# Kernel optimization log

Measured on AMD Instinct MI355X. Metric: run time of the kernel, lower is better.

## Reference

```python
import jax, jax.numpy as jnp
import numpy as np

FRAME, PROJ, MID, HID, T, B = 2048, 512, 128, 1024, 48, 512


def _uniform(key, shape, stdv):
    return jax.random.uniform(key, shape, jnp.float32, -stdv, stdv)


def setup_inputs() -> dict:
    key = jax.random.key(0)
    ks = jax.random.split(key, 16)
    sp = 1.0 / np.sqrt(FRAME)   # frame_embed init
    s1 = 1.0 / np.sqrt(HID)     # LSTMCell init (1/sqrt(hidden))
    sbd = 1.0 / np.sqrt(PROJ)   # BoundaryDetector init (1/sqrt(i_features))
    return {
        "video_feats": jax.random.normal(ks[0], (B, T, FRAME), jnp.float32),
        # frame_embed: Linear(frame_size, projected_size)
        "We": _uniform(ks[1], (PROJ, FRAME), sp),
        "be": _uniform(ks[2], (PROJ,), sp),
        # lstm1: LSTMCell(projected, hidden) with bias
        "W1_ih": _uniform(ks[3], (4 * HID, PROJ), s1),
        "W1_hh": _uniform(ks[4], (4 * HID, HID), s1),
        "b1_ih": _uniform(ks[5], (4 * HID,), s1),
        "b1_hh": _uniform(ks[6], (4 * HID,), s1),
        # lstm2: LSTMCell(hidden, hidden), bias=False
        "W2_ih": _uniform(ks[7], (4 * HID, HID), s1),
        "W2_hh": _uniform(ks[8], (4 * HID, HID), s1),
        # BoundaryDetector params
        "Wsi": _uniform(ks[9], (MID, PROJ), sbd),
        "Wsh": _uniform(ks[10], (MID, HID), sbd),
        "bbd": _uniform(ks[11], (MID,), sbd),
        "vs": _uniform(ks[12], (1, MID), sbd),
    }


def _lstm_cell(x, h, c, W_ih, W_hh, b):
    gates = x @ W_ih.T + h @ W_hh.T + b  # [B, 4H]
    i, f, g, o = jnp.split(gates, 4, axis=-1)  # PyTorch gate order i,f,g,o
    i, f, o = jax.nn.sigmoid(i), jax.nn.sigmoid(f), jax.nn.sigmoid(o)
    g = jnp.tanh(g)
    c_new = f * c + i * g
    h_new = o * jnp.tanh(c_new)
    return h_new, c_new


def _binary_gate(z):
    # eval mode: threshold 0.5; straight-through identity backward
    hard = (z > 0.5).astype(z.dtype)
    return z + jax.lax.stop_gradient(hard - z)


def reference(video_feats, We, be, W1_ih, W1_hh, b1_ih, b1_hh, W2_ih, W2_hh, Wsi, Wsh, bbd, vs):
    bsz = video_feats.shape[0]
    # frame embedding (dropout is identity in eval mode)
    v = video_feats @ We.T + be  # [B, T, PROJ]
    v_t = jnp.swapaxes(v, 0, 1)  # [T, B, PROJ]
    b1 = b1_ih + b1_hh
    zeros = jnp.zeros((bsz, HID), video_feats.dtype)

    def step(carry, vt):
        h1, c1, h2, c2 = carry
        z = jax.nn.sigmoid((vt @ Wsi.T + h1 @ Wsh.T + bbd) @ vs.T)  # [B, 1]
        s = _binary_gate(z)
        h1n, c1n = _lstm_cell(vt, h1, c1, W1_ih, W1_hh, b1)
        h2n, c2n = _lstm_cell(h1n * s, h2, c2, W2_ih, W2_hh, 0.0)
        h1n = h1n * (1.0 - s)
        c1n = c1n * (1.0 - s)
        return (h1n, c1n, h2n, c2n), None

    (h1, _, _, _), _ = jax.lax.scan(step, (zeros, zeros, zeros, zeros), v_t)
    return h1
```

## Files before the change

kernel.cpp:

```cpp
#include <hip/hip_runtime.h>

#define B_     512
#define T_     48
#define FRAME_ 2048
#define PROJ_  512
#define MID_   128
#define HID_   1024
#define G4_    4096

typedef unsigned short u16;
typedef __bf16 bf16x8 __attribute__((ext_vector_type(8)));
typedef float  f32x4  __attribute__((ext_vector_type(4)));

__device__ __forceinline__ float sigmoidf_(float x) {
    return 1.0f / (1.0f + expf(-x));
}
__device__ __forceinline__ u16 f2bf_rn(float f) {
    unsigned int u = __float_as_uint(f);
    u += 0x7fffu + ((u >> 16) & 1u);
    return (u16)(u >> 16);
}
__device__ __forceinline__ float bf2f(u16 s) {
    return __uint_as_float(((unsigned int)s) << 16);
}
__device__ __forceinline__ void gld16(const void* g, void* l) {
    __builtin_amdgcn_global_load_lds((const __attribute__((address_space(1))) void*)g,
                                     (__attribute__((address_space(3))) void*)l, 16, 0, 0);
}
__device__ __forceinline__ uint4 pack8(const u16* h) {
    return make_uint4((unsigned)h[0] | ((unsigned)h[1] << 16),
                      (unsigned)h[2] | ((unsigned)h[3] << 16),
                      (unsigned)h[4] | ((unsigned)h[5] << 16),
                      (unsigned)h[6] | ((unsigned)h[7] << 16));
}

__global__ void wvec_kernel(const float* __restrict__ Wsi, const float* __restrict__ Wsh,
                            const float* __restrict__ vs,
                            double* __restrict__ wsi_vd, float* __restrict__ wsh_v)
{
    const int gid = blockIdx.x * 256 + threadIdx.x;
    if (gid < 512) {
        double s = 0.0;
        for (int mi = 0; mi < MID_; ++mi)
            s += (double)vs[mi] * (double)Wsi[(size_t)mi * PROJ_ + gid];
        wsi_vd[gid] = s;
    } else if (gid < 1536) {
        const int k = gid - 512;
        double s = 0.0;
        for (int mi = 0; mi < MID_; ++mi)
            s += (double)vs[mi] * (double)Wsh[(size_t)mi * HID_ + k];
        wsh_v[k] = (float)s;
    }
}

__global__ void cc_kernel(const float* __restrict__ be, const double* __restrict__ wsi_vd,
                          const float* __restrict__ vs, const float* __restrict__ bbd,
                          double* __restrict__ cc)
{
    __shared__ double red[256];
    const int tid = threadIdx.x;
    double s = 0.0;
    for (int p = tid; p < PROJ_; p += 256) s += (double)be[p] * wsi_vd[p];
    red[tid] = s;
    __syncthreads();
    for (int st = 128; st > 0; st >>= 1) {
        if (tid < st) red[tid] += red[tid + st];
        __syncthreads();
    }
    if (tid == 0) {
        double b = 0.0;
        for (int mi = 0; mi < MID_; ++mi) b += (double)vs[mi] * (double)bbd[mi];
        cc[0] = red[0] + b;
    }
}

__global__ void u_kernel(const float* __restrict__ We, const double* __restrict__ wsi_vd,
                         double* __restrict__ u)
{
    const int f = blockIdx.x * 256 + threadIdx.x;
    double s = 0.0;
    for (int p = 0; p < PROJ_; ++p)
        s += wsi_vd[p] * (double)We[(size_t)p * FRAME_ + f];
    u[f] = s;
}

__global__ __launch_bounds__(256)
void vidpack_kernel(const float* __restrict__ video, const double* __restrict__ u,
                    const double* __restrict__ cc,
                    u16* __restrict__ phi, u16* __restrict__ plo,
                    float* __restrict__ Lv)
{
    __shared__ double red[16][17];
    const int tid = threadIdx.x;
    const int r   = tid & 15, kq = tid >> 4;
    const int row = blockIdx.x * 16 + r;
    const float* vr = video + (size_t)row * FRAME_;
    double s = 0.0;
#pragma unroll
    for (int j = 0; j < 16; ++j) {
        const int k0 = kq * 128 + j * 8;
        const float4 a = *(const float4*)&vr[k0];
        const float4 b = *(const float4*)&vr[k0 + 4];
        const float f[8] = {a.x, a.y, a.z, a.w, b.x, b.y, b.z, b.w};
        s += (double)f[0]*u[k0+0] + (double)f[1]*u[k0+1] + (double)f[2]*u[k0+2]
           + (double)f[3]*u[k0+3] + (double)f[4]*u[k0+4] + (double)f[5]*u[k0+5]
           + (double)f[6]*u[k0+6] + (double)f[7]*u[k0+7];
        u16 h[8], l[8];
#pragma unroll
        for (int e = 0; e < 8; ++e) {
            h[e] = f2bf_rn(f[e]);
            l[e] = f2bf_rn(f[e] - bf2f(h[e]));
        }
        const int g = kq * 16 + j;
        const size_t off = ((size_t)g * 24576 + row) * 16;
        *(uint4*)((char*)phi + off) = pack8(h);
        *(uint4*)((char*)plo + off) = pack8(l);
    }
    red[r][kq] = s;
    __syncthreads();
    if (tid < 16) {
        double t = 0.0;
#pragma unroll
        for (int q = 0; q < 16; ++q) t += red[tid][q];
        const int rw = blockIdx.x * 16 + tid;
        Lv[(rw % T_) * B_ + rw / T_] = (float)(t + cc[0]);
    }
}

__global__ void wepack_kernel(const float* __restrict__ We,
                              u16* __restrict__ phi, u16* __restrict__ plo)
{
    const int kk = blockIdx.x, by = blockIdx.y, tid = threadIdx.x;
#pragma unroll
    for (int pass = 0; pass < 2; ++pass) {
        const int g = tid + pass * 256;
        const int ko = g >> 7, n = g & 127;
        const int p = by * 128 + n;
        const int k = kk * 32 + ko * 8;
        const float4 a = *(const float4*)&We[(size_t)p * FRAME_ + k];
        const float4 b = *(const float4*)&We[(size_t)p * FRAME_ + k + 4];
        const float f[8] = {a.x, a.y, a.z, a.w, b.x, b.y, b.z, b.w};
        u16 h[8], l[8];
#pragma unroll
        for (int e = 0; e < 8; ++e) {
            h[e] = f2bf_rn(f[e]);
            l[e] = f2bf_rn(f[e] - bf2f(h[e]));
        }
        const size_t off = (((size_t)by * 64 + kk) * 512 + g) * 16;
        *(uint4*)((char*)phi + off) = pack8(h);
        *(uint4*)((char*)plo + off) = pack8(l);
    }
}

__global__ void wpack_kernel(const float* __restrict__ Wih, const float* __restrict__ Whh,
                             u16* __restrict__ phi, u16* __restrict__ plo)
{
    const int kk = blockIdx.x, by = blockIdx.y, tid = threadIdx.x;
#pragma unroll
    for (int pass = 0; pass < 2; ++pass) {
        const int g = tid + pass * 256;
        const int ko = g >> 7, n = g & 127;
        const int gate = n & 3, hl = n >> 2;
        const int srow = gate * HID_ + by * 32 + hl;
        const int k = kk * 32 + ko * 8;
        float4 a, b;
        if (k < 512) {
            a = *(const float4*)&Wih[(size_t)srow * PROJ_ + k];
            b = *(const float4*)&Wih[(size_t)srow * PROJ_ + k + 4];
        } else {
            a = *(const float4*)&Whh[(size_t)srow * HID_ + (k - 512)];
            b = *(const float4*)&Whh[(size_t)srow * HID_ + (k - 508)];
        }
        const float f[8] = {a.x, a.y, a.z, a.w, b.x, b.y, b.z, b.w};
        u16 h[8], l[8];
#pragma unroll
        for (int e = 0; e < 8; ++e) {
            h[e] = f2bf_rn(f[e]);
            l[e] = f2bf_rn(f[e] - bf2f(h[e]));
        }
        const size_t off = (((size_t)by * 48 + kk) * 512 + g) * 16;
        *(uint4*)((char*)phi + off) = pack8(h);
        *(uint4*)((char*)plo + off) = pack8(l);
    }
}

__global__ __launch_bounds__(512, 1)
void embed_mfma_kernel(const u16* __restrict__ Ahi_g, const u16* __restrict__ Alo_g,
                       const u16* __restrict__ Bhi_g, const u16* __restrict__ Blo_g,
                       const float* __restrict__ be,
                       u16* __restrict__ vphi, u16* __restrict__ vplo)
{
    __shared__ char smem[73728];
    const int tid = threadIdx.x;
    const int u_ = (blockIdx.x & 7) * 192 + (blockIdx.x >> 3);
    const int by = u_ / 384, bx = u_ % 384;
    const int n0 = by * 128;
    const int w = tid >> 6, l = tid & 63, lm = l & 15, ko4 = l >> 4;
    const int wr = (w >> 2) * 32, wc = (w & 3) * 32;
    const int t8 = tid & 255;
    const int koA = t8 >> 6, am = t8 & 63;

    const char* aV = (const char*)(tid < 256 ? Ahi_g : Alo_g)
                     + (size_t)koA * 393216 + ((size_t)bx * 64 + am) * 16;
    const char* bh = (const char*)Bhi_g + (size_t)by * 524288 + tid * 16;
    const char* bl = (const char*)Blo_g + (size_t)by * 524288 + tid * 16;

    auto stage = [&](int s, int buf) {
        char* base = smem + buf * 24576;
        gld16(aV + (size_t)s * 1572864, base + (tid >> 8) * 4096 + t8 * 16);
        gld16(bh + (size_t)s * 8192, base + 8192 + tid * 16);
        gld16(bl + (size_t)s * 8192, base + 16384 + tid * 16);
    };

    f32x4 acc[2][2] = {};
    stage(0, 0);
    stage(1, 1);
    for (int kk = 0; kk < 64; ++kk) {
        const int cb = kk % 3;
        if (kk + 2 < 64) {
            stage(kk + 2, (kk + 2) % 3);
            asm volatile("s_waitcnt vmcnt(6)" ::: "memory");
        } else if (kk + 1 < 64) {
            asm volatile("s_waitcnt vmcnt(3)" ::: "memory");
        } else {
            asm volatile("s_waitcnt vmcnt(0)" ::: "memory");
        }
        __builtin_amdgcn_sched_barrier(0);
        __builtin_amdgcn_s_barrier();

        const char* rb = smem + cb * 24576;
        bf16x8 fAh[2], fAl[2], fBh[2], fBl[2];
#pragma unroll
        for (int mt = 0; mt < 2; ++mt) {
            const int idx = ko4 * 64 + wr + mt * 16 + lm;
            fAh[mt] = *(const bf16x8*)(rb + idx * 16);
            fAl[mt] = *(const bf16x8*)(rb + 4096 + idx * 16);
        }
#pragma unroll
        for (int nt = 0; nt < 2; ++nt) {
            const int idx = ko4 * 128 + wc + nt * 16 + lm;
            fBh[nt] = *(const bf16x8*)(rb + 8192 + idx * 16);
            fBl[nt] = *(const bf16x8*)(rb + 16384 + idx * 16);
        }
        asm volatile("s_waitcnt lgkmcnt(0)" ::: "memory");
        __builtin_amdgcn_sched_barrier(0);
        __builtin_amdgcn_s_barrier();
        __builtin_amdgcn_s_setprio(1);
#pragma unroll
        for (int mt = 0; mt < 2; ++mt)
#pragma unroll
            for (int nt = 0; nt < 2; ++nt) {
                acc[mt][nt] = __builtin_amdgcn_mfma_f32_16x16x32_bf16(fAh[mt], fBh[nt], acc[mt][nt], 0, 0, 0);
                acc[mt][nt] = __builtin_amdgcn_mfma_f32_16x16x32_bf16(fAh[mt], fBl[nt], acc[mt][nt], 0, 0, 0);
                acc[mt][nt] = __builtin_amdgcn_mfma_f32_16x16x32_bf16(fAl[mt], fBh[nt], acc[mt][nt], 0, 0, 0);
            }
        __builtin_amdgcn_s_setprio(0);
    }

    __syncthreads();
    float* S = (float*)smem;
#pragma unroll
    for (int mt = 0; mt < 2; ++mt)
#pragma unroll
        for (int nt = 0; nt < 2; ++nt) {
            const int col = wc + nt * 16 + lm;
#pragma unroll
            for (int r = 0; r < 4; ++r) {
                const int row = wr + mt * 16 + ko4 * 4 + r;
                S[row * 132 + col] = acc[mt][nt][r];
            }
        }
    __syncthreads();

#pragma unroll
    for (int pass = 0; pass < 2; ++pass) {
        const int pidx = tid + pass * 512;
        const int m = pidx >> 4, gr = pidx & 15;
        const int p0 = n0 + gr * 8;
        const float4 s0 = *(const float4*)&S[m * 132 + gr * 8];
        const float4 s1 = *(const float4*)&S[m * 132 + gr * 8 + 4];
        const float4 e0 = *(const float4*)&be[p0];
        const float4 e1 = *(const float4*)&be[p0 + 4];
        const float o[8] = {s0.x + e0.x, s0.y + e0.y, s0.z + e0.z, s0.w + e0.w,
                            s1.x + e1.x, s1.y + e1.y, s1.z + e1.z, s1.w + e1.w};
        u16 h[8], lo[8];
#pragma unroll
        for (int e = 0; e < 8; ++e) {
            h[e] = f2bf_rn(o[e]);
            lo[e] = f2bf_rn(o[e] - bf2f(h[e]));
        }
        const int R = bx * 64 + m;
        const int t = R % T_, b = R / T_;
        const size_t off = (size_t)t * 524288 + (((size_t)(p0 >> 3)) * 512 + b) * 16;
        *(uint4*)((char*)vphi + off) = pack8(h);
        *(uint4*)((char*)vplo + off) = pack8(lo);
    }
}

__global__ __launch_bounds__(512, 1)
void lstm_mfma_kernel(const u16* __restrict__ vthi, const u16* __restrict__ vtlo,
                      const u16* __restrict__ hhi,  const u16* __restrict__ hlo,
                      const u16* __restrict__ Whi,  const u16* __restrict__ Wlo,
                      const float* __restrict__ b1,
                      const float* __restrict__ Lv_t,
                      const float* __restrict__ Pin,
                      float* __restrict__ Pout,
                      const float* __restrict__ wsh_v,
                      float* __restrict__ c1, float* __restrict__ h1o,
                      u16* __restrict__ hhio, u16* __restrict__ hloo)
{
    __shared__ char smem[73984];
    float* keepsm = (float*)(smem + 73728);
    const int tid = threadIdx.x;
    const int bid = blockIdx.x;
    const int xcd = bid & 7, slot = bid >> 3;
    const int by  = xcd * 4 + (slot & 3);
    const int bx  = slot >> 2;
    const int b0  = bx * 64;
    const int w = tid >> 6, l = tid & 63, lm = l & 15, ko4 = l >> 4;
    const int wr = (w >> 2) * 32, wc = (w & 3) * 32;
    const int t8 = tid & 255;
    const int koA = t8 >> 6, am = t8 & 63;

    const char* aV = (const char*)(tid < 256 ? vthi : vtlo)
                     + koA * 8192 + (b0 + am) * 16;
    const char* aH = (const char*)(tid < 256 ? hhi : hlo)
                     + koA * 8192 + (b0 + am) * 16;
    const char* bh = (const char*)Whi + (size_t)by * 393216 + tid * 16;
    const char* bl = (const char*)Wlo + (size_t)by * 393216 + tid * 16;

    auto stage = [&](int s, int buf) {
        char* base = smem + buf * 24576;
        const char* asrc = (s < 16) ? aV + s * 32768 : aH + (s - 16) * 32768;
        gld16(asrc, base + (tid >> 8) * 4096 + t8 * 16);
        gld16(bh + s * 8192, base + 8192 + tid * 16);
        gld16(bl + s * 8192, base + 16384 + tid * 16);
    };

    f32x4 acc[2][2] = {};
    stage(0, 0);
    stage(1, 1);

    if (tid < 64) {
        double s = (double)Lv_t[b0 + tid];
#pragma unroll
        for (int j = 0; j < 32; ++j) s += (double)Pin[j * B_ + b0 + tid];
        keepsm[tid] = (s > 0.0) ? 0.0f : 1.0f;
    }

    for (int kk = 0; kk < 48; ++kk) {
        const int cb = kk % 3;
        if (kk + 2 < 48) {
            stage(kk + 2, (kk + 2) % 3);
            asm volatile("s_waitcnt vmcnt(6)" ::: "memory");
        } else if (kk + 1 < 48) {
            asm volatile("s_waitcnt vmcnt(3)" ::: "memory");
        } else {
            asm volatile("s_waitcnt vmcnt(0)" ::: "memory");
        }
        __builtin_amdgcn_sched_barrier(0);
        __builtin_amdgcn_s_barrier();

        const char* rb = smem + cb * 24576;
        bf16x8 fAh[2], fAl[2], fBh[2], fBl[2];
#pragma unroll
        for (int mt = 0; mt < 2; ++mt) {
            const int idx = ko4 * 64 + wr + mt * 16 + lm;
            fAh[mt] = *(const bf16x8*)(rb + idx * 16);
            fAl[mt] = *(const bf16x8*)(rb + 4096 + idx * 16);
        }
#pragma unroll
        for (int nt = 0; nt < 2; ++nt) {
            const int idx = ko4 * 128 + wc + nt * 16 + lm;
            fBh[nt] = *(const bf16x8*)(rb + 8192 + idx * 16);
            fBl[nt] = *(const bf16x8*)(rb + 16384 + idx * 16);
        }
        asm volatile("s_waitcnt lgkmcnt(0)" ::: "memory");
        __builtin_amdgcn_sched_barrier(0);
        __builtin_amdgcn_s_barrier();
        __builtin_amdgcn_s_setprio(1);
#pragma unroll
        for (int mt = 0; mt < 2; ++mt)
#pragma unroll
            for (int nt = 0; nt < 2; ++nt) {
                acc[mt][nt] = __builtin_amdgcn_mfma_f32_16x16x32_bf16(fAh[mt], fBh[nt], acc[mt][nt], 0, 0, 0);
                acc[mt][nt] = __builtin_amdgcn_mfma_f32_16x16x32_bf16(fAh[mt], fBl[nt], acc[mt][nt], 0, 0, 0);
                acc[mt][nt] = __builtin_amdgcn_mfma_f32_16x16x32_bf16(fAl[mt], fBh[nt], acc[mt][nt], 0, 0, 0);
            }
        __builtin_amdgcn_s_setprio(0);
    }

    __syncthreads();
    float* S = (float*)smem;
#pragma unroll
    for (int mt = 0; mt < 2; ++mt)
#pragma unroll
        for (int nt = 0; nt < 2; ++nt) {
            const int col = wc + nt * 16 + lm;
#pragma unroll
            for (int r = 0; r < 4; ++r) {
                const int row = wr + mt * 16 + ko4 * 4 + r;
                S[row * 132 + col] = acc[mt][nt][r];
            }
        }
    __syncthreads();

    const int h_l = tid & 31, rg = tid >> 5;
    const int hg  = by * 32 + h_l;
    const float bI = b1[hg], bF = b1[HID_ + hg], bG = b1[2 * HID_ + hg], bO = b1[3 * HID_ + hg];
    const float wv = wsh_v[hg];
    const size_t hgbase = (((size_t)by * 4 + (h_l >> 3)) * 512) * 16 + (h_l & 7) * 2;
#pragma unroll
    for (int i = 0; i < 4; ++i) {
        const int m = rg * 4 + i;
        const int b = b0 + m;
        const float4 g4 = *(const float4*)&S[m * 132 + h_l * 4];
        const float i_ = sigmoidf_(g4.x + bI);
        const float f_ = sigmoidf_(g4.y + bF);
        const float g_ = tanhf(g4.z + bG);
        const float o_ = sigmoidf_(g4.w + bO);
        const size_t off = (size_t)b * HID_ + hg;
        float cn = f_ * c1[off] + i_ * g_;
        float hn = o_ * tanhf(cn);
        const float kp = keepsm[m];
        cn *= kp; hn *= kp;
        c1[off] = cn;
        if (h1o) h1o[off] = hn;
        const u16 hb = f2bf_rn(hn);
        const size_t hoff = hgbase + (size_t)b * 16;
        *(u16*)((char*)hhio + hoff) = hb;
        *(u16*)((char*)hloo + hoff) = f2bf_rn(hn - bf2f(hb));
        float pr = hn * wv;
        pr += __shfl_xor(pr, 16);
        pr += __shfl_xor(pr, 8);
        pr += __shfl_xor(pr, 4);
        pr += __shfl_xor(pr, 2);
        pr += __shfl_xor(pr, 1);
        if (h_l == 0) Pout[by * B_ + b] = pr;
    }
}

__global__ void b1sum_kernel(const float* __restrict__ bih,
                             const float* __restrict__ bhh,
                             float* __restrict__ b1)
{
    const int i = blockIdx.x * 256 + threadIdx.x;
    if (i < G4_) b1[i] = bih[i] + bhh[i];
}

extern "C" void kernel_launch(void* const* d_in, const int* in_sizes, int n_in,
                              void* d_out, int out_size, void* d_ws, size_t ws_size,
                              hipStream_t stream)
{
    const float* video = (const float*)d_in[0];
    const float* We    = (const float*)d_in[1];
    const float* be    = (const float*)d_in[2];
    const float* W1_ih = (const float*)d_in[3];
    const float* W1_hh = (const float*)d_in[4];
    const float* b1_ih = (const float*)d_in[5];
    const float* b1_hh = (const float*)d_in[6];
    const float* Wsi   = (const float*)d_in[9];
    const float* Wsh   = (const float*)d_in[10];
    const float* bbd   = (const float*)d_in[11];
    const float* vs    = (const float*)d_in[12];
    float* out = (float*)d_out;

    char* p = (char*)d_ws;
    auto alloc = [&](size_t bytes) { char* r = p; p += (bytes + 255) & ~(size_t)255; return r; };
    u16* vidhi = (u16*)alloc((size_t)24576 * FRAME_ * 2);
    u16* vidlo = (u16*)alloc((size_t)24576 * FRAME_ * 2);
    u16* vphi  = (u16*)alloc((size_t)T_ * B_ * PROJ_ * 2);
    u16* vplo  = (u16*)alloc((size_t)T_ * B_ * PROJ_ * 2);
    u16* Wehi  = (u16*)alloc((size_t)PROJ_ * FRAME_ * 2);
    u16* Welo  = (u16*)alloc((size_t)PROJ_ * FRAME_ * 2);
    u16* Whi   = (u16*)alloc((size_t)G4_ * 1536 * 2);
    u16* Wlo   = (u16*)alloc((size_t)G4_ * 1536 * 2);
    float* c1  = (float*)alloc((size_t)B_ * HID_ * 4);
    u16* hhiA  = (u16*)alloc((size_t)B_ * HID_ * 2);
    u16* hhiB  = (u16*)alloc((size_t)B_ * HID_ * 2);
    u16* hloA  = (u16*)alloc((size_t)B_ * HID_ * 2);
    u16* hloB  = (u16*)alloc((size_t)B_ * HID_ * 2);
    double* wsi_vd = (double*)alloc(512 * 8);
    double* ud     = (double*)alloc(2048 * 8);
    double* ccd    = (double*)alloc(256);
    float* wsh_v = (float*)alloc(1024 * 4);
    float* Lv    = (float*)alloc((size_t)T_ * B_ * 4);
    float* PA    = (float*)alloc(32 * B_ * 4);
    float* PB    = (float*)alloc(32 * B_ * 4);
    float* b1    = (float*)alloc(G4_ * 4);

    hipMemsetAsync(c1,   0, (size_t)B_ * HID_ * 4, stream);
    hipMemsetAsync(hhiA, 0, (size_t)B_ * HID_ * 2, stream);
    hipMemsetAsync(hloA, 0, (size_t)B_ * HID_ * 2, stream);
    hipMemsetAsync(PA,   0, 32 * B_ * 4, stream);

    b1sum_kernel<<<16, 256, 0, stream>>>(b1_ih, b1_hh, b1);
    wvec_kernel<<<6, 256, 0, stream>>>(Wsi, Wsh, vs, wsi_vd, wsh_v);
    cc_kernel<<<1, 256, 0, stream>>>(be, wsi_vd, vs, bbd, ccd);
    u_kernel<<<8, 256, 0, stream>>>(We, wsi_vd, ud);
    wepack_kernel<<<dim3(64, 4), 256, 0, stream>>>(We, Wehi, Welo);
    wpack_kernel<<<dim3(48, 32), 256, 0, stream>>>(W1_ih, W1_hh, Whi, Wlo);
    vidpack_kernel<<<1536, 256, 0, stream>>>(video, ud, ccd, vidhi, vidlo, Lv);
    embed_mfma_kernel<<<1536, 512, 0, stream>>>(vidhi, vidlo, Wehi, Welo, be, vphi, vplo);

    u16* hhi_in = hhiA; u16* hhi_out = hhiB;
    u16* hlo_in = hloA; u16* hlo_out = hloB;
    float* Pin = PA; float* Pout = PB;

    for (int t = 0; t < T_; ++t) {
        const u16* vthi = vphi + (size_t)t * 262144;
        const u16* vtlo = vplo + (size_t)t * 262144;
        float* ho = (t == T_ - 1) ? out : nullptr;
        lstm_mfma_kernel<<<256, 512, 0, stream>>>(vthi, vtlo, hhi_in, hlo_in,
                                                  Whi, Wlo, b1,
                                                  Lv + t * B_, Pin, Pout, wsh_v,
                                                  c1, ho, hhi_out, hlo_out);
        { u16* tmp = hhi_in; hhi_in = hhi_out; hhi_out = tmp; }
        { u16* tmp = hlo_in; hlo_in = hlo_out; hlo_out = tmp; }
        { float* tmp = Pin; Pin = Pout; Pout = tmp; }
    }
}
```

Baseline: 1.699 ms.

## Hoist input-to-hidden LSTM projection out of recurrence into one batched GEMM

Splits the LSTM weight packing into separate W_ih and W_hh buffers and adds a gx_mfma kernel that computes x_t·W_ih^T plus bias for all 48 timesteps at once into a large fp32 Gx buffer. Each recurrent step then runs only the 1024-deep hidden GEMM and adds the precomputed Gx slice in the epilogue. The aim is to move a third of the serial per-step work into one highly parallel GEMM, at the cost of about 400 MB of extra Gx writes and reads. The embed and LSTM pipelines are also changed to issue the next stage load after the fragment reads and to drop one barrier per iteration, and the embed block-to-tile mapping is changed.

```diff
diff --git a/kernel.cpp b/kernel.cpp
--- a/kernel.cpp
+++ b/kernel.cpp
@@ -152,8 +152,8 @@
     }
 }
 
-__global__ void wpack_kernel(const float* __restrict__ Wih, const float* __restrict__ Whh,
-                             u16* __restrict__ phi, u16* __restrict__ plo)
+__global__ void wihpack_kernel(const float* __restrict__ Wih,
+                               u16* __restrict__ phi, u16* __restrict__ plo)
 {
     const int kk = blockIdx.x, by = blockIdx.y, tid = threadIdx.x;
 #pragma unroll
@@ -163,14 +163,8 @@
         const int gate = n & 3, hl = n >> 2;
         const int srow = gate * HID_ + by * 32 + hl;
         const int k = kk * 32 + ko * 8;
-        float4 a, b;
-        if (k < 512) {
-            a = *(const float4*)&Wih[(size_t)srow * PROJ_ + k];
-            b = *(const float4*)&Wih[(size_t)srow * PROJ_ + k + 4];
-        } else {
-            a = *(const float4*)&Whh[(size_t)srow * HID_ + (k - 512)];
-            b = *(const float4*)&Whh[(size_t)srow * HID_ + (k - 508)];
-        }
+        const float4 a = *(const float4*)&Wih[(size_t)srow * PROJ_ + k];
+        const float4 b = *(const float4*)&Wih[(size_t)srow * PROJ_ + k + 4];
         const float f[8] = {a.x, a.y, a.z, a.w, b.x, b.y, b.z, b.w};
         u16 h[8], l[8];
 #pragma unroll
@@ -178,10 +172,46 @@
             h[e] = f2bf_rn(f[e]);
             l[e] = f2bf_rn(f[e] - bf2f(h[e]));
         }
-        const size_t off = (((size_t)by * 48 + kk) * 512 + g) * 16;
+        const size_t off = (((size_t)by * 16 + kk) * 512 + g) * 16;
         *(uint4*)((char*)phi + off) = pack8(h);
         *(uint4*)((char*)plo + off) = pack8(l);
     }
+}
+
+__global__ void whhpack_kernel(const float* __restrict__ Whh,
+                               u16* __restrict__ phi, u16* __restrict__ plo)
+{
+    const int kk = blockIdx.x, by = blockIdx.y, tid = threadIdx.x;
+#pragma unroll
+    for (int pass = 0; pass < 2; ++pass) {
+        const int g = tid + pass * 256;
+        const int ko = g >> 7, n = g & 127;
+        const int gate = n & 3, hl = n >> 2;
+        const int srow = gate * HID_ + by * 32 + hl;
+        const int k = kk * 32 + ko * 8;
+        const float4 a = *(const float4*)&Whh[(size_t)srow * HID_ + k];
+        const float4 b = *(const float4*)&Whh[(size_t)srow * HID_ + k + 4];
+        const float f[8] = {a.x, a.y, a.z, a.w, b.x, b.y, b.z, b.w};
+        u16 h[8], l[8];
+#pragma unroll
+        for (int e = 0; e < 8; ++e) {
+            h[e] = f2bf_rn(f[e]);
+            l[e] = f2bf_rn(f[e] - bf2f(h[e]));
+        }
+        const size_t off = (((size_t)by * 32 + kk) * 512 + g) * 16;
+        *(uint4*)((char*)phi + off) = pack8(h);
+        *(uint4*)((char*)plo + off) = pack8(l);
+    }
+}
+
+__global__ void b1g_kernel(const float* __restrict__ bih, const float* __restrict__ bhh,
+                           float* __restrict__ b1g)
+{
+    const int n = blockIdx.x * 256 + threadIdx.x;
+    const int by = n >> 7, nl = n & 127;
+    const int gate = nl & 3, hl = nl >> 2;
+    const int src = gate * HID_ + by * 32 + hl;
+    b1g[n] = bih[src] + bhh[src];
 }
 
 __global__ __launch_bounds__(512, 1)
@@ -192,8 +222,8 @@
 {
     __shared__ char smem[73728];
     const int tid = threadIdx.x;
-    const int u_ = (blockIdx.x & 7) * 192 + (blockIdx.x >> 3);
-    const int by = u_ / 384, bx = u_ % 384;
+    const int xcd = blockIdx.x & 7, s_ = blockIdx.x >> 3;
+    const int by = s_ & 3, bx = xcd * 48 + (s_ >> 2);
     const int n0 = by * 128;
     const int w = tid >> 6, l = tid & 63, lm = l & 15, ko4 = l >> 4;
     const int wr = (w >> 2) * 32, wc = (w & 3) * 32;
@@ -216,19 +246,12 @@
     stage(0, 0);
     stage(1, 1);
     for (int kk = 0; kk < 64; ++kk) {
-        const int cb = kk % 3;
-        if (kk + 2 < 64) {
-            stage(kk + 2, (kk + 2) % 3);
-            asm volatile("s_waitcnt vmcnt(6)" ::: "memory");
-        } else if (kk + 1 < 64) {
-            asm volatile("s_waitcnt vmcnt(3)" ::: "memory");
-        } else {
-            asm volatile("s_waitcnt vmcnt(0)" ::: "memory");
-        }
+        if (kk < 63) asm volatile("s_waitcnt vmcnt(3)" ::: "memory");
+        else         asm volatile("s_waitcnt vmcnt(0)" ::: "memory");
         __builtin_amdgcn_sched_barrier(0);
         __builtin_amdgcn_s_barrier();
 
-        const char* rb = smem + cb * 24576;
+        const char* rb = smem + (kk % 3) * 24576;
         bf16x8 fAh[2], fAl[2], fBh[2], fBl[2];
 #pragma unroll
         for (int mt = 0; mt < 2; ++mt) {
@@ -242,9 +265,9 @@
             fBh[nt] = *(const bf16x8*)(rb + 8192 + idx * 16);
             fBl[nt] = *(const bf16x8*)(rb + 16384 + idx * 16);
         }
+        if (kk + 2 < 64) stage(kk + 2, (kk + 2) % 3);
         asm volatile("s_waitcnt lgkmcnt(0)" ::: "memory");
         __builtin_amdgcn_sched_barrier(0);
-        __builtin_amdgcn_s_barrier();
         __builtin_amdgcn_s_setprio(1);
 #pragma unroll
         for (int mt = 0; mt < 2; ++mt)
@@ -298,10 +321,105 @@
 }
 
 __global__ __launch_bounds__(512, 1)
-void lstm_mfma_kernel(const u16* __restrict__ vthi, const u16* __restrict__ vtlo,
-                      const u16* __restrict__ hhi,  const u16* __restrict__ hlo,
-                      const u16* __restrict__ Whi,  const u16* __restrict__ Wlo,
-                      const float* __restrict__ b1,
+void gx_mfma_kernel(const u16* __restrict__ vphi, const u16* __restrict__ vplo,
+                    const u16* __restrict__ Wihhi, const u16* __restrict__ Wihlo,
+                    const float* __restrict__ b1g, float* __restrict__ Gx)
+{
+    __shared__ char smem[73728];
+    const int tid = threadIdx.x;
+    const int by = blockIdx.x & 31;
+    const int tb = blockIdx.x >> 5;
+    const int t = tb >> 3, bx = tb & 7;
+    const int b0 = bx * 64, n0 = by * 128;
+    const int w = tid >> 6, l = tid & 63, lm = l & 15, ko4 = l >> 4;
+    const int wr = (w >> 2) * 32, wc = (w & 3) * 32;
+    const int t8 = tid & 255;
+    const int koA = t8 >> 6, am = t8 & 63;
+
+    const char* aV = (const char*)(tid < 256 ? vphi : vplo)
+                     + (size_t)t * 524288 + ((size_t)koA * 512 + b0 + am) * 16;
+    const char* bh = (const char*)Wihhi + (size_t)by * 131072 + tid * 16;
+    const char* bl = (const char*)Wihlo + (size_t)by * 131072 + tid * 16;
+
+    auto stage = [&](int s, int buf) {
+        char* base = smem + buf * 24576;
+        gld16(aV + s * 32768, base + (tid >> 8) * 4096 + t8 * 16);
+        gld16(bh + s * 8192, base + 8192 + tid * 16);
+        gld16(bl + s * 8192, base + 16384 + tid * 16);
+    };
+
+    f32x4 acc[2][2] = {};
+    stage(0, 0);
+    stage(1, 1);
+    for (int kk = 0; kk < 16; ++kk) {
+        if (kk < 15) asm volatile("s_waitcnt vmcnt(3)" ::: "memory");
+        else         asm volatile("s_waitcnt vmcnt(0)" ::: "memory");
+        __builtin_amdgcn_sched_barrier(0);
+        __builtin_amdgcn_s_barrier();
+
+        const char* rb = smem + (kk % 3) * 24576;
+        bf16x8 fAh[2], fAl[2], fBh[2], fBl[2];
+#pragma unroll
+        for (int mt = 0; mt < 2; ++mt) {
+            const int idx = ko4 * 64 + wr + mt * 16 + lm;
+            fAh[mt] = *(const bf16x8*)(rb + idx * 16);
+            fAl[mt] = *(const bf16x8*)(rb + 4096 + idx * 16);
+        }
+#pragma unroll
+        for (int nt = 0; nt < 2; ++nt) {
+            const int idx = ko4 * 128 + wc + nt * 16 + lm;
+            fBh[nt] = *(const bf16x8*)(rb + 8192 + idx * 16);
+            fBl[nt] = *(const bf16x8*)(rb + 16384 + idx * 16);
+        }
+        if (kk + 2 < 16) stage(kk + 2, (kk + 2) % 3);
+        asm volatile("s_waitcnt lgkmcnt(0)" ::: "memory");
+        __builtin_amdgcn_sched_barrier(0);
+        __builtin_amdgcn_s_setprio(1);
+#pragma unroll
+        for (int mt = 0; mt < 2; ++mt)
+#pragma unroll
+            for (int nt = 0; nt < 2; ++nt) {
+                acc[mt][nt] = __builtin_amdgcn_mfma_f32_16x16x32_bf16(fAh[mt], fBh[nt], acc[mt][nt], 0, 0, 0);
+                acc[mt][nt] = __builtin_amdgcn_mfma_f32_16x16x32_bf16(fAh[mt], fBl[nt], acc[mt][nt], 0, 0, 0);
+                acc[mt][nt] = __builtin_amdgcn_mfma_f32_16x16x32_bf16(fAl[mt], fBh[nt], acc[mt][nt], 0, 0, 0);
+            }
+        __builtin_amdgcn_s_setprio(0);
+    }
+
+    __syncthreads();
+    float* S = (float*)smem;
+#pragma unroll
+    for (int mt = 0; mt < 2; ++mt)
+#pragma unroll
+        for (int nt = 0; nt < 2; ++nt) {
+            const int col = wc + nt * 16 + lm;
+#pragma unroll
+            for (int r = 0; r < 4; ++r) {
+                const int row = wr + mt * 16 + ko4 * 4 + r;
+                S[row * 132 + col] = acc[mt][nt][r];
+            }
+        }
+    __syncthreads();
+
+#pragma unroll
+    for (int pass = 0; pass < 2; ++pass) {
+        const int pidx = tid + pass * 512;
+        const int m = pidx >> 4, gr = pidx & 15;
+        const int c0 = gr * 8;
+        const float4 s0 = *(const float4*)&S[m * 132 + c0];
+        const float4 s1 = *(const float4*)&S[m * 132 + c0 + 4];
+        const float4 a0 = *(const float4*)&b1g[n0 + c0];
+        const float4 a1 = *(const float4*)&b1g[n0 + c0 + 4];
+        float* dst = Gx + ((size_t)t * 512 + b0 + m) * 4096 + n0 + c0;
+        *(float4*)dst       = make_float4(s0.x + a0.x, s0.y + a0.y, s0.z + a0.z, s0.w + a0.w);
+        *(float4*)(dst + 4) = make_float4(s1.x + a1.x, s1.y + a1.y, s1.z + a1.z, s1.w + a1.w);
+    }
+}
+
+__global__ __launch_bounds__(512, 1)
+void lstm_mfma_kernel(const u16* __restrict__ hhi,  const u16* __restrict__ hlo,
+                      const u16* __restrict__ Whhhi, const u16* __restrict__ Whhlo,
+                      const float* __restrict__ Gxt,
                       const float* __restrict__ Lv_t,
                       const float* __restrict__ Pin,
                       float* __restrict__ Pout,
@@ -322,17 +440,14 @@
     const int t8 = tid & 255;
     const int koA = t8 >> 6, am = t8 & 63;
 
-    const char* aV = (const char*)(tid < 256 ? vthi : vtlo)
-                     + koA * 8192 + (b0 + am) * 16;
     const char* aH = (const char*)(tid < 256 ? hhi : hlo)
-                     + koA * 8192 + (b0 + am) * 16;
-    const char* bh = (const char*)Whi + (size_t)by * 393216 + tid * 16;
-    const char* bl = (const char*)Wlo + (size_t)by * 393216 + tid * 16;
+                     + ((size_t)koA * 512 + b0 + am) * 16;
+    const char* bh = (const char*)Whhhi + (size_t)by * 262144 + tid * 16;
+    const char* bl = (const char*)Whhlo + (size_t)by * 262144 + tid * 16;
 
     auto stage = [&](int s, int buf) {
         char* base = smem + buf * 24576;
-        const char* asrc = (s < 16) ? aV + s * 32768 : aH + (s - 16) * 32768;
-        gld16(asrc, base + (tid >> 8) * 4096 + t8 * 16);
+        gld16(aH + s * 32768, base + (tid >> 8) * 4096 + t8 * 16);
         gld16(bh + s * 8192, base + 8192 + tid * 16);
         gld16(bl + s * 8192, base + 16384 + tid * 16);
     };
@@ -348,20 +463,13 @@
         keepsm[tid] = (s > 0.0) ? 0.0f : 1.0f;
     }
 
-    for (int kk = 0; kk < 48; ++kk) {
-        const int cb = kk % 3;
-        if (kk + 2 < 48) {
-            stage(kk + 2, (kk + 2) % 3);
-            asm volatile("s_waitcnt vmcnt(6)" ::: "memory");
-        } else if (kk + 1 < 48) {
-            asm volatile("s_waitcnt vmcnt(3)" ::: "memory");
-        } else {
-            asm volatile("s_waitcnt vmcnt(0)" ::: "memory");
-        }
+    for (int kk = 0; kk < 32; ++kk) {
+        if (kk < 31) asm volatile("s_waitcnt vmcnt(3)" ::: "memory");
+        else         asm volatile("s_waitcnt vmcnt(0)" ::: "memory");
         __builtin_amdgcn_sched_barrier(0);
         __builtin_amdgcn_s_barrier();
 
-        const char* rb = smem + cb * 24576;
+        const char* rb = smem + (kk % 3) * 24576;
         bf16x8 fAh[2], fAl[2], fBh[2], fBl[2];
 #pragma unroll
         for (int mt = 0; mt < 2; ++mt) {
@@ -375,9 +483,9 @@
             fBh[nt] = *(const bf16x8*)(rb + 8192 + idx * 16);
             fBl[nt] = *(const bf16x8*)(rb + 16384 + idx * 16);
         }
+        if (kk + 2 < 32) stage(kk + 2, (kk + 2) % 3);
         asm volatile("s_waitcnt lgkmcnt(0)" ::: "memory");
         __builtin_amdgcn_sched_barrier(0);
-        __builtin_amdgcn_s_barrier();
         __builtin_amdgcn_s_setprio(1);
 #pragma unroll
         for (int mt = 0; mt < 2; ++mt)
@@ -390,6 +498,13 @@
         __builtin_amdgcn_s_setprio(0);
     }
 
+    const int h_l = tid & 31, rg = tid >> 5;
+    const int hg  = by * 32 + h_l;
+    float4 gx[4];
+#pragma unroll
+    for (int i = 0; i < 4; ++i)
+        gx[i] = *(const float4*)&Gxt[((size_t)b0 + rg * 4 + i) * 4096 + by * 128 + h_l * 4];
+
     __syncthreads();
     float* S = (float*)smem;
 #pragma unroll
@@ -405,9 +520,6 @@
         }
     __syncthreads();
 
-    const int h_l = tid & 31, rg = tid >> 5;
-    const int hg  = by * 32 + h_l;
-    const float bI = b1[hg], bF = b1[HID_ + hg], bG = b1[2 * HID_ + hg], bO = b1[3 * HID_ + hg];
     const float wv = wsh_v[hg];
     const size_t hgbase = (((size_t)by * 4 + (h_l >> 3)) * 512) * 16 + (h_l & 7) * 2;
 #pragma unroll
@@ -415,10 +527,10 @@
         const int m = rg * 4 + i;
         const int b = b0 + m;
         const float4 g4 = *(const float4*)&S[m * 132 + h_l * 4];
-        const float i_ = sigmoidf_(g4.x + bI);
-        const float f_ = sigmoidf_(g4.y + bF);
-        const float g_ = tanhf(g4.z + bG);
-        const float o_ = sigmoidf_(g4.w + bO);
+        const float i_ = sigmoidf_(g4.x + gx[i].x);
+        const float f_ = sigmoidf_(g4.y + gx[i].y);
+        const float g_ = tanhf(g4.z + gx[i].z);
+        const float o_ = sigmoidf_(g4.w + gx[i].w);
         const size_t off = (size_t)b * HID_ + hg;
         float cn = f_ * c1[off] + i_ * g_;
         float hn = o_ * tanhf(cn);
@@ -440,14 +552,6 @@
     }
 }
 
-__global__ void b1sum_kernel(const float* __restrict__ bih,
-                             const float* __restrict__ bhh,
-                             float* __restrict__ b1)
-{
-    const int i = blockIdx.x * 256 + threadIdx.x;
-    if (i < G4_) b1[i] = bih[i] + bhh[i];
-}
-
 extern "C" void kernel_launch(void* const* d_in, const int* in_sizes, int n_in,
                               void* d_out, int out_size, void* d_ws, size_t ws_size,
                               hipStream_t stream)
@@ -473,8 +577,11 @@
     u16* vplo  = (u16*)alloc((size_t)T_ * B_ * PROJ_ * 2);
     u16* Wehi  = (u16*)alloc((size_t)PROJ_ * FRAME_ * 2);
     u16* Welo  = (u16*)alloc((size_t)PROJ_ * FRAME_ * 2);
-    u16* Whi   = (u16*)alloc((size_t)G4_ * 1536 * 2);
-    u16* Wlo   = (u16*)alloc((size_t)G4_ * 1536 * 2);
+    u16* Wihhi = (u16*)alloc((size_t)G4_ * PROJ_ * 2);
+    u16* Wihlo = (u16*)alloc((size_t)G4_ * PROJ_ * 2);
+    u16* Whhhi = (u16*)alloc((size_t)G4_ * HID_ * 2);
+    u16* Whhlo = (u16*)alloc((size_t)G4_ * HID_ * 2);
+    float* Gx  = (float*)alloc((size_t)T_ * B_ * G4_ * 4);
     float* c1  = (float*)alloc((size_t)B_ * HID_ * 4);
     u16* hhiA  = (u16*)alloc((size_t)B_ * HID_ * 2);
     u16* hhiB  = (u16*)alloc((size_t)B_ * HID_ * 2);
@@ -487,32 +594,32 @@
     float* Lv    = (float*)alloc((size_t)T_ * B_ * 4);
     float* PA    = (float*)alloc(32 * B_ * 4);
     float* PB    = (float*)alloc(32 * B_ * 4);
-    float* b1    = (float*)alloc(G4_ * 4);
+    float* b1g   = (float*)alloc(G4_ * 4);
 
     hipMemsetAsync(c1,   0, (size_t)B_ * HID_ * 4, stream);
     hipMemsetAsync(hhiA, 0, (size_t)B_ * HID_ * 2, stream);
     hipMemsetAsync(hloA, 0, (size_t)B_ * HID_ * 2, stream);
     hipMemsetAsync(PA,   0, 32 * B_ * 4, stream);
 
-    b1sum_kernel<<<16, 256, 0, stream>>>(b1_ih, b1_hh, b1);
+    b1g_kernel<<<16, 256, 0, stream>>>(b1_ih, b1_hh, b1g);
     wvec_kernel<<<6, 256, 0, stream>>>(Wsi, Wsh, vs, wsi_vd, wsh_v);
     cc_kernel<<<1, 256, 0, stream>>>(be, wsi_vd, vs, bbd, ccd);
     u_kernel<<<8, 256, 0, stream>>>(We, wsi_vd, ud);
     wepack_kernel<<<dim3(64, 4), 256, 0, stream>>>(We, Wehi, Welo);
-    wpack_kernel<<<dim3(48, 32), 256, 0, stream>>>(W1_ih, W1_hh, Whi, Wlo);
+    wihpack_kernel<<<dim3(16, 32), 256, 0, stream>>>(W1_ih, Wihhi, Wihlo);
+    whhpack_kernel<<<dim3(32, 32), 256, 0, stream>>>(W1_hh, Whhhi, Whhlo);
     vidpack_kernel<<<1536, 256, 0, stream>>>(video, ud, ccd, vidhi, vidlo, Lv);
     embed_mfma_kernel<<<1536, 512, 0, stream>>>(vidhi, vidlo, Wehi, Welo, be, vphi, vplo);
+    gx_mfma_kernel<<<12288, 512, 0, stream>>>(vphi, vplo, Wihhi, Wihlo, b1g, Gx);
 
     u16* hhi_in = hhiA; u16* hhi_out = hhiB;
     u16* hlo_in = hloA; u16* hlo_out = hloB;
     float* Pin = PA; float* Pout = PB;
 
     for (int t = 0; t < T_; ++t) {
-        const u16* vthi = vphi + (size_t)t * 262144;
-        const u16* vtlo = vplo + (size_t)t * 262144;
         float* ho = (t == T_ - 1) ? out : nullptr;
-        lstm_mfma_kernel<<<256, 512, 0, stream>>>(vthi, vtlo, hhi_in, hlo_in,
-                                                  Whi, Wlo, b1,
+        lstm_mfma_kernel<<<256, 512, 0, stream>>>(hhi_in, hlo_in, Whhhi, Whhlo,
+                                                  Gx + (size_t)t * B_ * G4_,
                                                   Lv + t * B_, Pin, Pout, wsh_v,
                                                   c1, ho, hhi_out, hlo_out);
         { u16* tmp = hhi_in; hhi_in = hhi_out; hhi_out = tmp; }
```

After: 1.664 ms. 1.02x faster.
